# Kernel optimization log

Measured on AMD Instinct MI355X. Metric: run time of the kernel, lower is better.

Reference implementation:

```python
import jax, jax.numpy as jnp
import numpy as np

IN_F, OUT_F, N_CH, N_TILES, PTS = 256, 256, 1024, 1024, 256
OMEGA = 30.0


def setup_inputs() -> dict:
    key = jax.random.key(0)
    kx, kw, kb, ki = jax.random.split(key, 4)
    bound = float(np.sqrt(6.0 / IN_F) / OMEGA)  # SIREN-style init (is_first=False)
    x = jax.random.normal(kx, (N_TILES, PTS, IN_F), dtype=jnp.float32)
    weight = jax.random.uniform(kw, (N_CH, IN_F, OUT_F), dtype=jnp.float32,
                                minval=-bound, maxval=bound)
    bias = jax.random.uniform(kb, (1, 1, OUT_F), dtype=jnp.float32,
                              minval=-bound, maxval=bound)
    indices = jax.random.randint(ki, (N_TILES,), 0, N_CH, dtype=jnp.int64)
    return {"x": x, "weight": weight, "bias": bias, "indices": indices}


def reference(x, weight, bias, indices):
    # gather per-tile weight slice then batched matmul: [T,P,I] @ [T,I,O] -> [T,P,O]
    w = weight[indices]                      # [T, I, O]
    out = jnp.einsum('tpi,tio->tpo', x, w) + bias[0]
    return jnp.sin(OMEGA * out)
```

## Files before the change

### kernel.cpp

```cpp
#include <hip/hip_runtime.h>

typedef _Float16 half8_t __attribute__((ext_vector_type(8)));
typedef _Float16 half4_t __attribute__((ext_vector_type(4)));
typedef float    float4_t __attribute__((ext_vector_type(4)));

#define N_TILES 1024
#define PTS     256
#define IN_F    256
#define OUT_F   256
#define BM      64
#define BK      32
#define LDK     40
#define NSTEP   (IN_F / BK)
#define OMEGA_C 30.0f

#define BARRIER() do {                                        \
    asm volatile("s_waitcnt lgkmcnt(0)" ::: "memory");        \
    __builtin_amdgcn_s_barrier();                             \
    asm volatile("" ::: "memory");                            \
  } while (0)

#define BSWZ(g, n) (((g) ^ (((n) >> 3) & 3)))

__global__ __launch_bounds__(512, 4)
void siren_tile_gemm(const float* __restrict__ x,
                     const float* __restrict__ w,
                     const float* __restrict__ bias,
                     const void* __restrict__ idx_raw,
                     float* __restrict__ out) {
  __shared__ __align__(16) _Float16 Al[2][BM][LDK];
  __shared__ __align__(16) _Float16 Bl[2][OUT_F][LDK];

  const int tid = threadIdx.x;

  const int b    = blockIdx.x;
  const int xcd  = b & 7;
  const int rest = b >> 3;
  const int tile = xcd + 8 * (rest >> 2);
  const int mq   = rest & 3;

  const int hiw  = ((const int*)idx_raw)[2 * (tid & 63) + 1];
  const bool is32 = __any(hiw != 0);
  const int ch = is32 ? ((const int*)idx_raw)[tile]
                      : (int)(((const long long*)idx_raw)[tile]);

  const float* __restrict__ Xg = x + (size_t)tile * (PTS * IN_F) + (size_t)mq * BM * IN_F;
  const float* __restrict__ Wg = w + (size_t)ch * (IN_F * OUT_F);
  float*       __restrict__ Og = out + (size_t)tile * (PTS * OUT_F) + (size_t)mq * BM * OUT_F;

  const int a_row = tid >> 3;
  const int a_col = (tid & 7) * 4;
  const int b_kb  = tid >> 6;
  const int b_nb  = tid & 63;

  float4_t acc[2][4];
#pragma unroll
  for (int m = 0; m < 2; ++m)
#pragma unroll
    for (int n = 0; n < 4; ++n)
      acc[m][n] = (float4_t){0.f, 0.f, 0.f, 0.f};

  float4_t aS[2];
  float4_t bS[2][4];

#define ISSUE(slot, s)                                                          \
  do {                                                                          \
    const int k0_ = (s) * BK;                                                   \
    aS[slot] = *(const float4_t*)(Xg + (size_t)a_row * IN_F + k0_ + a_col);     \
    _Pragma("unroll")                                                           \
    for (int j = 0; j < 4; ++j)                                                 \
      bS[slot][j] = *(const float4_t*)(Wg + (size_t)(k0_ + b_kb * 4 + j) * OUT_F + b_nb * 4); \
  } while (0)

#define STORE_LDS(slot, buf)                                                    \
  do {                                                                          \
    half4_t ha_ = {(_Float16)aS[slot].x, (_Float16)aS[slot].y,                  \
                   (_Float16)aS[slot].z, (_Float16)aS[slot].w};                 \
    *(half4_t*)&Al[buf][a_row][a_col] = ha_;                                    \
    _Pragma("unroll")                                                           \
    for (int i = 0; i < 4; ++i) {                                               \
      const int n_ = b_nb * 4 + i;                                              \
      half4_t hb_ = {(_Float16)bS[slot][0][i], (_Float16)bS[slot][1][i],        \
                     (_Float16)bS[slot][2][i], (_Float16)bS[slot][3][i]};       \
      *(half4_t*)&Bl[buf][n_][BSWZ(b_kb >> 1, n_) * 8 + (b_kb & 1) * 4] = hb_;  \
    }                                                                           \
  } while (0)

  ISSUE(0, 0);
  ISSUE(1, 1);
  STORE_LDS(0, 0);
  BARRIER();

  const int lane = tid & 63;
  const int wid  = tid >> 6;
  const int wm   = (wid >> 2) * 32;
  const int wn   = (wid & 3) * 64;
  const int fr   = lane & 15;
  const int kg   = lane >> 4;

#pragma unroll
  for (int s = 0; s < NSTEP; ++s) {
    const int cur = s & 1;

    half8_t af[2], bf[4];
#pragma unroll
    for (int m = 0; m < 2; ++m)
      af[m] = *(const half8_t*)&Al[cur][wm + m * 16 + fr][kg * 8];
#pragma unroll
    for (int n = 0; n < 4; ++n) {
      const int r = wn + n * 16 + fr;
      bf[n] = *(const half8_t*)&Bl[cur][r][BSWZ(kg, r) * 8];
    }

#pragma unroll
    for (int m = 0; m < 2; ++m)
#pragma unroll
      for (int n = 0; n < 4; ++n)
        acc[m][n] = __builtin_amdgcn_mfma_f32_16x16x32_f16(af[m], bf[n], acc[m][n], 0, 0, 0);

    if (s + 2 < NSTEP) ISSUE(cur, s + 2);
    if (s + 1 < NSTEP) {
      STORE_LDS(cur ^ 1, cur ^ 1);
      BARRIER();
    }
  }

  float bv[4];
#pragma unroll
  for (int n = 0; n < 4; ++n) bv[n] = OMEGA_C * bias[wn + n * 16 + fr];

#pragma unroll
  for (int m = 0; m < 2; ++m) {
#pragma unroll
    for (int n = 0; n < 4; ++n) {
#pragma unroll
      for (int j = 0; j < 4; ++j) {
        const int row = wm + m * 16 + kg * 4 + j;
        const int col = wn + n * 16 + fr;
        Og[(size_t)row * OUT_F + col] = __sinf(fmaf(OMEGA_C, acc[m][n][j], bv[n]));
      }
    }
  }
}

extern "C" void kernel_launch(void* const* d_in, const int* in_sizes, int n_in,
                              void* d_out, int out_size, void* d_ws, size_t ws_size,
                              hipStream_t stream) {
  const float* x    = (const float*)d_in[0];
  const float* w    = (const float*)d_in[1];
  const float* bias = (const float*)d_in[2];
  const void*  idx  = d_in[3];
  float*       out  = (float*)d_out;

  siren_tile_gemm<<<N_TILES * 4, 512, 0, stream>>>(x, w, bias, idx, out);
}
```

Measured before the change: 166.2 us.

## Convert tile GEMM to persistent kernel with full-K X staging and cross-unit prefetch

The kernel now launches 512 persistent blocks, and each block walks 8 consecutive 64-row work units instead of one block per unit. Each unit stages the whole 64x256 X slice in LDS once and splits the output into two 128-column halves, streaming the weights in 64-deep K chunks. The next unit's X rows and first weight chunk are prefetched during the current unit's last steps and epilogue. This is meant to hide global latency and launch/tail overhead, at the cost of more LDS per block (lower occupancy), a heavier XOR-swizzle scheme, and tighter sequential dependencies inside each block.

Result: slower. 315.4 us (+89.8%).

```diff
diff --git a/kernel.cpp b/kernel.cpp
--- a/kernel.cpp
+++ b/kernel.cpp
@@ -4,14 +4,6 @@
 typedef _Float16 half4_t __attribute__((ext_vector_type(4)));
 typedef float    float4_t __attribute__((ext_vector_type(4)));
 
-#define N_TILES 1024
-#define PTS     256
-#define IN_F    256
-#define OUT_F   256
-#define BM      64
-#define BK      32
-#define LDK     40
-#define NSTEP   (IN_F / BK)
 #define OMEGA_C 30.0f
 
 #define BARRIER() do {                                        \
@@ -20,126 +12,192 @@
     asm volatile("" ::: "memory");                            \
   } while (0)
 
-#define BSWZ(g, n) (((g) ^ (((n) >> 3) & 3)))
+#define W_ISSUE(dst, wgp, sW)                                                   \
+  do {                                                                          \
+    _Pragma("unroll")                                                           \
+    for (int j_ = 0; j_ < 4; ++j_)                                              \
+      dst[j_] = *(const float4_t*)((wgp) + (size_t)((sW) * 64 + kq * 4 + j_) * 256 + nq * 4); \
+  } while (0)
+
+#define W_STORE(src, buf)                                                       \
+  do {                                                                          \
+    _Pragma("unroll")                                                           \
+    for (int ii_ = 0; ii_ < 4; ++ii_) {                                         \
+      const int ip_ = (ii_ + nq) & 3;                                           \
+      const int n_  = nq * 4 + ip_;                                             \
+      half4_t hb_ = {(_Float16)src[0][ip_], (_Float16)src[1][ip_],              \
+                     (_Float16)src[2][ip_], (_Float16)src[3][ip_]};             \
+      const int pg_ = (kq >> 1) ^ (n_ & 7) ^ (2 * ((n_ >> 5) & 3));             \
+      *(half4_t*)&Wl[buf][n_ * 64 + pg_ * 8 + (kq & 1) * 4] = hb_;              \
+    }                                                                           \
+  } while (0)
+
+#define X_ISSUE(xgp, hb)                                                        \
+  do {                                                                          \
+    _Pragma("unroll")                                                           \
+    for (int j_ = 0; j_ < 4; ++j_)                                              \
+      xr[j_] = *(const float4_t*)((xgp) + (size_t)(xrow + (hb) + j_) * 256 + lane * 4); \
+  } while (0)
+
+#define X_COMMIT(hb)                                                            \
+  do {                                                                          \
+    _Pragma("unroll")                                                           \
+    for (int j_ = 0; j_ < 4; ++j_) {                                            \
+      const int r_ = xrow + (hb) + j_;                                          \
+      half4_t hx_ = {(_Float16)xr[j_].x, (_Float16)xr[j_].y,                    \
+                     (_Float16)xr[j_].z, (_Float16)xr[j_].w};                   \
+      const int pg_ = (lane >> 1) ^ (r_ & 7) ^ (2 * ((lane >> 4) & 3));         \
+      *(half4_t*)&Xl[r_ * 256 + pg_ * 8 + (lane & 1) * 4] = hx_;                \
+    }                                                                           \
+  } while (0)
+
+#define STEP(sS, buf)                                                           \
+  do {                                                                          \
+    _Pragma("unroll")                                                           \
+    for (int h_ = 0; h_ < 2; ++h_) {                                            \
+      half8_t af_[2], bf_[2];                                                   \
+      _Pragma("unroll")                                                         \
+      for (int m_ = 0; m_ < 2; ++m_) {                                          \
+        const int r_ = wm + m_ * 16 + fr;                                       \
+        const int u_ = (h_ * 4 + kg) ^ (fr & 7) ^ (2 * ((sS) & 3));             \
+        af_[m_] = *(const half8_t*)&Xl[r_ * 256 + ((sS) * 8 + u_) * 8];         \
+      }                                                                         \
+      _Pragma("unroll")                                                         \
+      for (int n_ = 0; n_ < 2; ++n_) {                                          \
+        const int r_ = wn + n_ * 16 + fr;                                       \
+        const int g_ = (h_ * 4 + kg) ^ (r_ & 7) ^ (2 * ((r_ >> 5) & 3));        \
+        bf_[n_] = *(const half8_t*)&Wl[buf][r_ * 64 + g_ * 8];                  \
+      }                                                                         \
+      _Pragma("unroll")                                                         \
+      for (int m_ = 0; m_ < 2; ++m_)                                            \
+        _Pragma("unroll")                                                       \
+        for (int n_ = 0; n_ < 2; ++n_)                                          \
+          acc[m_][n_] = __builtin_amdgcn_mfma_f32_16x16x32_f16(af_[m_], bf_[n_], acc[m_][n_], 0, 0, 0); \
+    }                                                                           \
+  } while (0)
+
+#define ACC_ZERO()                                                              \
+  do {                                                                          \
+    _Pragma("unroll")                                                           \
+    for (int m_ = 0; m_ < 2; ++m_)                                              \
+      _Pragma("unroll")                                                         \
+      for (int n_ = 0; n_ < 2; ++n_)                                            \
+        acc[m_][n_] = (float4_t){0.f, 0.f, 0.f, 0.f};                           \
+  } while (0)
+
+#define EPILOGUE(ogp, nhv)                                                      \
+  do {                                                                          \
+    _Pragma("unroll")                                                           \
+    for (int m_ = 0; m_ < 2; ++m_)                                              \
+      _Pragma("unroll")                                                         \
+      for (int n_ = 0; n_ < 2; ++n_)                                            \
+        _Pragma("unroll")                                                       \
+        for (int j_ = 0; j_ < 4; ++j_) {                                        \
+          const int row_ = wm + m_ * 16 + kg * 4 + j_;                          \
+          const int col_ = wn + n_ * 16 + fr;                                   \
+          (ogp)[(size_t)row_ * 256 + col_] =                                    \
+              __sinf(fmaf(OMEGA_C, acc[m_][n_][j_], bv[nhv][n_]));              \
+        }                                                                       \
+  } while (0)
 
 __global__ __launch_bounds__(512, 4)
-void siren_tile_gemm(const float* __restrict__ x,
-                     const float* __restrict__ w,
-                     const float* __restrict__ bias,
-                     const void* __restrict__ idx_raw,
-                     float* __restrict__ out) {
-  __shared__ __align__(16) _Float16 Al[2][BM][LDK];
-  __shared__ __align__(16) _Float16 Bl[2][OUT_F][LDK];
-
-  const int tid = threadIdx.x;
-
-  const int b    = blockIdx.x;
-  const int xcd  = b & 7;
-  const int rest = b >> 3;
-  const int tile = xcd + 8 * (rest >> 2);
-  const int mq   = rest & 3;
-
-  const int hiw  = ((const int*)idx_raw)[2 * (tid & 63) + 1];
-  const bool is32 = __any(hiw != 0);
-  const int ch = is32 ? ((const int*)idx_raw)[tile]
-                      : (int)(((const long long*)idx_raw)[tile]);
-
-  const float* __restrict__ Xg = x + (size_t)tile * (PTS * IN_F) + (size_t)mq * BM * IN_F;
-  const float* __restrict__ Wg = w + (size_t)ch * (IN_F * OUT_F);
-  float*       __restrict__ Og = out + (size_t)tile * (PTS * OUT_F) + (size_t)mq * BM * OUT_F;
-
-  const int a_row = tid >> 3;
-  const int a_col = (tid & 7) * 4;
-  const int b_kb  = tid >> 6;
-  const int b_nb  = tid & 63;
-
-  float4_t acc[2][4];
-#pragma unroll
-  for (int m = 0; m < 2; ++m)
-#pragma unroll
-    for (int n = 0; n < 4; ++n)
-      acc[m][n] = (float4_t){0.f, 0.f, 0.f, 0.f};
-
-  float4_t aS[2];
-  float4_t bS[2][4];
-
-#define ISSUE(slot, s)                                                          \
-  do {                                                                          \
-    const int k0_ = (s) * BK;                                                   \
-    aS[slot] = *(const float4_t*)(Xg + (size_t)a_row * IN_F + k0_ + a_col);     \
-    _Pragma("unroll")                                                           \
-    for (int j = 0; j < 4; ++j)                                                 \
-      bS[slot][j] = *(const float4_t*)(Wg + (size_t)(k0_ + b_kb * 4 + j) * OUT_F + b_nb * 4); \
-  } while (0)
-
-#define STORE_LDS(slot, buf)                                                    \
-  do {                                                                          \
-    half4_t ha_ = {(_Float16)aS[slot].x, (_Float16)aS[slot].y,                  \
-                   (_Float16)aS[slot].z, (_Float16)aS[slot].w};                 \
-    *(half4_t*)&Al[buf][a_row][a_col] = ha_;                                    \
-    _Pragma("unroll")                                                           \
-    for (int i = 0; i < 4; ++i) {                                               \
-      const int n_ = b_nb * 4 + i;                                              \
-      half4_t hb_ = {(_Float16)bS[slot][0][i], (_Float16)bS[slot][1][i],        \
-                     (_Float16)bS[slot][2][i], (_Float16)bS[slot][3][i]};       \
-      *(half4_t*)&Bl[buf][n_][BSWZ(b_kb >> 1, n_) * 8 + (b_kb & 1) * 4] = hb_;  \
-    }                                                                           \
-  } while (0)
-
-  ISSUE(0, 0);
-  ISSUE(1, 1);
-  STORE_LDS(0, 0);
-  BARRIER();
-
+void siren_persist(const float* __restrict__ x,
+                   const float* __restrict__ wgt,
+                   const float* __restrict__ bias,
+                   const void* __restrict__ idx_raw,
+                   float* __restrict__ out) {
+  __shared__ _Float16 Xl[64 * 256];
+  __shared__ _Float16 Wl[2][128 * 64];
+
+  const int tid  = threadIdx.x;
   const int lane = tid & 63;
   const int wid  = tid >> 6;
-  const int wm   = (wid >> 2) * 32;
-  const int wn   = (wid & 3) * 64;
-  const int fr   = lane & 15;
-  const int kg   = lane >> 4;
-
+
+  const int hiw   = ((const int*)idx_raw)[2 * lane + 1];
+  const bool is32 = __any(hiw != 0);
+  const int* idx32       = (const int*)idx_raw;
+  const long long* idx64 = (const long long*)idx_raw;
+
+  const int fr = lane & 15, kg = lane >> 4;
+  const int wm = (wid >> 2) * 32;
+  const int wn = (wid & 3) * 32;
+  const int nq = tid & 31, kq = tid >> 5;
+  const int xrow = wid * 8;
+
+  const int ubase = (blockIdx.x & 7) * 512 + (blockIdx.x >> 3) * 8;
+
+  float bv[2][2];
 #pragma unroll
-  for (int s = 0; s < NSTEP; ++s) {
-    const int cur = s & 1;
-
-    half8_t af[2], bf[4];
+  for (int h = 0; h < 2; ++h)
 #pragma unroll
-    for (int m = 0; m < 2; ++m)
-      af[m] = *(const half8_t*)&Al[cur][wm + m * 16 + fr][kg * 8];
-#pragma unroll
-    for (int n = 0; n < 4; ++n) {
-      const int r = wn + n * 16 + fr;
-      bf[n] = *(const half8_t*)&Bl[cur][r][BSWZ(kg, r) * 8];
+    for (int n = 0; n < 2; ++n)
+      bv[h][n] = OMEGA_C * bias[h * 128 + wn + n * 16 + fr];
+
+  int ch_cur;
+  { const int t0 = ubase >> 2; ch_cur = is32 ? idx32[t0] : (int)idx64[t0]; }
+
+  float4_t xr[4], wvA[4], wvB[4];
+
+  {
+    const float* Xg0 = x + (size_t)(ubase >> 2) * 65536 + (size_t)(ubase & 3) * 16384;
+    X_ISSUE(Xg0, 0);
+    X_COMMIT(0);
+    X_ISSUE(Xg0, 4);
+    const float* Wg0 = wgt + (size_t)ch_cur * 65536;
+    W_ISSUE(wvA, Wg0, 0);
+  }
+
+#pragma unroll 1
+  for (int u = 0; u < 8; ++u) {
+    const int uw   = ubase + u;
+    const int tile = uw >> 2, mq = uw & 3;
+    const float* Wg = wgt + (size_t)ch_cur * 65536;
+    float* Og = out + (size_t)tile * 65536 + (size_t)mq * 16384;
+
+    int ch_next = ch_cur;
+    if (u < 7) {
+      const int tn = (uw + 1) >> 2;
+      ch_next = is32 ? idx32[tn] : (int)idx64[tn];
     }
 
-#pragma unroll
-    for (int m = 0; m < 2; ++m)
-#pragma unroll
-      for (int n = 0; n < 4; ++n)
-        acc[m][n] = __builtin_amdgcn_mfma_f32_16x16x32_f16(af[m], bf[n], acc[m][n], 0, 0, 0);
-
-    if (s + 2 < NSTEP) ISSUE(cur, s + 2);
-    if (s + 1 < NSTEP) {
-      STORE_LDS(cur ^ 1, cur ^ 1);
-      BARRIER();
+    float4_t acc[2][2];
+    ACC_ZERO();
+
+    X_COMMIT(4);
+    W_ISSUE(wvB, Wg, 1);
+    W_STORE(wvA, 0);
+    BARRIER();
+    STEP(0, 0);  W_ISSUE(wvA, Wg, 2);        W_STORE(wvB, 1);  BARRIER();
+    STEP(1, 1);  W_ISSUE(wvB, Wg, 3);        W_STORE(wvA, 0);  BARRIER();
+    STEP(2, 0);  W_ISSUE(wvA, Wg + 128, 0);  W_STORE(wvB, 1);  BARRIER();
+    STEP(3, 1);  BARRIER();
+    W_ISSUE(wvB, Wg + 128, 1);
+    W_STORE(wvA, 0);
+    EPILOGUE(Og, 0);
+    BARRIER();
+    ACC_ZERO();
+    STEP(0, 0);  W_ISSUE(wvA, Wg + 128, 2);  W_STORE(wvB, 1);  BARRIER();
+    STEP(1, 1);  W_ISSUE(wvB, Wg + 128, 3);  W_STORE(wvA, 0);  BARRIER();
+    STEP(2, 0);
+    if (u < 7) {
+      const int un = uw + 1;
+      const float* Xgn = x + (size_t)(un >> 2) * 65536 + (size_t)(un & 3) * 16384;
+      X_ISSUE(Xgn, 0);
+      __builtin_amdgcn_sched_barrier(0);
     }
-  }
-
-  float bv[4];
-#pragma unroll
-  for (int n = 0; n < 4; ++n) bv[n] = OMEGA_C * bias[wn + n * 16 + fr];
-
-#pragma unroll
-  for (int m = 0; m < 2; ++m) {
-#pragma unroll
-    for (int n = 0; n < 4; ++n) {
-#pragma unroll
-      for (int j = 0; j < 4; ++j) {
-        const int row = wm + m * 16 + kg * 4 + j;
-        const int col = wn + n * 16 + fr;
-        Og[(size_t)row * OUT_F + col] = __sinf(fmaf(OMEGA_C, acc[m][n][j], bv[n]));
-      }
+    W_STORE(wvB, 1);
+    BARRIER();
+    STEP(3, 1);  BARRIER();
+    if (u < 7) {
+      const int un = uw + 1;
+      const float* Xgn = x + (size_t)(un >> 2) * 65536 + (size_t)(un & 3) * 16384;
+      X_COMMIT(0);
+      X_ISSUE(Xgn, 4);
+      const float* Wgn = wgt + (size_t)ch_next * 65536;
+      W_ISSUE(wvA, Wgn, 0);
     }
+    EPILOGUE(Og + 128, 1);
+    ch_cur = ch_next;
   }
 }
 
@@ -152,5 +210,5 @@
   const void*  idx  = d_in[3];
   float*       out  = (float*)d_out;
 
-  siren_tile_gemm<<<N_TILES * 4, 512, 0, stream>>>(x, w, bias, idx, out);
+  siren_persist<<<512, 512, 0, stream>>>(x, w, bias, idx, out);
 }
```
